# Kernel optimization log

Hardware: AMD Instinct MI355X
Metric: run time of the kernel (lower is better)

## Reference

```python
import jax, jax.numpy as jnp
import numpy as np

B, T, D, E = 8, 512, 128, 256

def setup_inputs() -> dict:
    key = jax.random.key(0)
    ks = jax.random.split(key, 6)
    s_d = 1.0 / np.sqrt(D)
    return {
        "x": jax.random.normal(ks[0], (B, T, D), jnp.float32),
        "Wg": jax.random.normal(ks[1], (D, E), jnp.float32) * s_d,
        "bg": jnp.zeros((E,), jnp.float32),
        "expert_w": jax.random.normal(ks[2], (E, D, D), jnp.float32) * s_d,
        "w1": jax.random.normal(ks[3], (D, D), jnp.float32) * s_d,
        "b1": jnp.zeros((D,), jnp.float32),
        "w2": jax.random.normal(ks[4], (D, D), jnp.float32) * s_d,
        "b2": jnp.zeros((D,), jnp.float32),
    }

def reference(x, Wg, bg, expert_w, w1, b1, w2, b2):
    n_experts = expert_w.shape[0]
    # router (context=None -> route on x itself)
    gate_scores = jax.nn.softmax(x @ Wg + bg, axis=-1)            # [B,T,E]
    top_vals, top_idx = jax.lax.top_k(gate_scores, 2)             # [B,T,2]
    top_w = top_vals / (jnp.sum(top_vals, axis=-1, keepdims=True) + 1e-6)
    # dense per-expert projection (faithful to original einsum over ALL experts)
    expert_outputs = jnp.einsum('btd,edo->bteo', x, expert_w)     # [B,T,E,D]
    # top-2 one-hot mask with normalized weights -> [B,T,E]
    mask = jnp.sum(jax.nn.one_hot(top_idx, n_experts, dtype=x.dtype) * top_w[..., None], axis=2)
    mixed = jnp.einsum('bteo,bte->bto', expert_outputs, mask)     # [B,T,D]
    # SwiGLU
    g = mixed @ w1 + b1
    weighted_avg = g * jax.nn.sigmoid(g) * (mixed @ w2 + b2)      # [B,T,D]
    # variance consensus against swiglu output
    diff_sq = jnp.square(expert_outputs - weighted_avg[:, :, None, :])
    weighted_var = jnp.einsum('bteo,bte->bto', diff_sq, mask)     # [B,T,D]
    consensus = jnp.exp(-jnp.mean(weighted_var, axis=-1))         # [B,T]
    return weighted_avg, consensus
```

## Files before the change

### kernel.cpp

```cpp
#include <hip/hip_runtime.h>
#include <math.h>

#define NT  4096
#define DD  128
#define EE  256
#define CAP 2048

__global__ __launch_bounds__(256) void logits_kernel(
    const float* __restrict__ x, const float* __restrict__ Wg,
    const float* __restrict__ bg, float* __restrict__ logits,
    int* __restrict__ cnt)
{
    const int bid = blockIdx.x;
    const int tid = threadIdx.x;
    if (bid == 0) cnt[tid] = 0;

    __shared__ float xt[DD][8];

    {
        const int q = tid >> 5, part = tid & 31;
        const float4 v = *(reinterpret_cast<const float4*>(
            x + (size_t)(bid * 8 + q) * DD) + part);
        xt[part * 4 + 0][q] = v.x;
        xt[part * 4 + 1][q] = v.y;
        xt[part * 4 + 2][q] = v.z;
        xt[part * 4 + 3][q] = v.w;
    }
    __syncthreads();

    const int e = tid;
    const float be = bg[e];
    float a0 = be, a1 = be, a2 = be, a3 = be;
    float a4 = be, a5 = be, a6 = be, a7 = be;
    #pragma unroll 8
    for (int d = 0; d < DD; ++d) {
        const float w = Wg[(size_t)d * EE + e];
        const float4 xa = *reinterpret_cast<const float4*>(&xt[d][0]);
        const float4 xb = *reinterpret_cast<const float4*>(&xt[d][4]);
        a0 = fmaf(xa.x, w, a0);  a1 = fmaf(xa.y, w, a1);
        a2 = fmaf(xa.z, w, a2);  a3 = fmaf(xa.w, w, a3);
        a4 = fmaf(xb.x, w, a4);  a5 = fmaf(xb.y, w, a5);
        a6 = fmaf(xb.z, w, a6);  a7 = fmaf(xb.w, w, a7);
    }
    float* lr = logits + (size_t)(bid * 8) * EE + e;
    lr[0 * EE] = a0;  lr[1 * EE] = a1;  lr[2 * EE] = a2;  lr[3 * EE] = a3;
    lr[4 * EE] = a4;  lr[5 * EE] = a5;  lr[6 * EE] = a6;  lr[7 * EE] = a7;
}

__global__ __launch_bounds__(256) void top2_kernel(
    const float* __restrict__ logits, float2* __restrict__ w_out,
    int* __restrict__ cnt, int* __restrict__ plist)
{
    const int lane = threadIdx.x & 63;
    const int t    = blockIdx.x * 4 + (threadIdx.x >> 6);
    const float4 lg = *reinterpret_cast<const float4*>(logits + (size_t)t * EE + lane * 4);
    float v[4] = {lg.x, lg.y, lg.z, lg.w};

    float m = v[0]; int mi = lane * 4;
    #pragma unroll
    for (int j = 1; j < 4; ++j)
        if (v[j] > m) { m = v[j]; mi = lane * 4 + j; }
    #pragma unroll
    for (int s = 32; s; s >>= 1) {
        const float om = __shfl_xor(m, s);
        const int   oi = __shfl_xor(mi, s);
        if (om > m || (om == m && oi < mi)) { m = om; mi = oi; }
    }

    float ssum = 0.0f;
    #pragma unroll
    for (int j = 0; j < 4; ++j) ssum += __expf(v[j] - m);
    #pragma unroll
    for (int s = 32; s; s >>= 1) ssum += __shfl_xor(ssum, s);

    float m2 = -INFINITY; int mi2 = 0;
    #pragma unroll
    for (int j = 0; j < 4; ++j) {
        const int ei = lane * 4 + j;
        if (ei != mi && v[j] > m2) { m2 = v[j]; mi2 = ei; }
    }
    #pragma unroll
    for (int s = 32; s; s >>= 1) {
        const float om = __shfl_xor(m2, s);
        const int   oi = __shfl_xor(mi2, s);
        if (om > m2 || (om == m2 && oi < mi2)) { m2 = om; mi2 = oi; }
    }

    if (lane == 0) {
        const float p1 = 1.0f / ssum;
        const float p2 = __expf(m2 - m) / ssum;
        const float den = p1 + p2 + 1e-6f;
        w_out[t] = make_float2(p1 / den, p2 / den);
        const int pos1 = atomicAdd(&cnt[mi], 1);
        if (pos1 < CAP) plist[mi * CAP + pos1] = t * 2;
        const int pos2 = atomicAdd(&cnt[mi2], 1);
        if (pos2 < CAP) plist[mi2 * CAP + pos2] = t * 2 + 1;
    }
}

__global__ __launch_bounds__(128) void expert_kernel(
    const float* __restrict__ x, const float* __restrict__ ew,
    const int* __restrict__ cnt, const int* __restrict__ plist,
    float* __restrict__ ybuf)
{
    const int wg = (blockIdx.x & 7) * 256 + (blockIdx.x >> 3);
    const int e  = wg >> 3;
    const int c  = wg & 7;
    int n = cnt[e];
    if (n > CAP) n = CAP;
    if (n <= c) return;

    const int o   = threadIdx.x;
    const int* pl = plist + e * CAP;
    const float* W = ew + (size_t)e * DD * DD;

    __shared__ float xt[DD][8];
    __shared__ int   fis[8];

    for (int base = c; base < n; base += 64) {
        {
            const int q = o >> 4, part = o & 15;
            if (base + q * 8 < n) {
                const int fi = pl[base + q * 8];
                if (part == 0) fis[q] = fi;
                const float4* xr = reinterpret_cast<const float4*>(
                    x + (size_t)(fi >> 1) * DD) + part * 2;
                const float4 u0 = xr[0], u1 = xr[1];
                xt[part * 8 + 0][q] = u0.x;  xt[part * 8 + 1][q] = u0.y;
                xt[part * 8 + 2][q] = u0.z;  xt[part * 8 + 3][q] = u0.w;
                xt[part * 8 + 4][q] = u1.x;  xt[part * 8 + 5][q] = u1.y;
                xt[part * 8 + 6][q] = u1.z;  xt[part * 8 + 7][q] = u1.w;
            }
        }
        __syncthreads();

        float a0 = 0.f, a1 = 0.f, a2 = 0.f, a3 = 0.f;
        float a4 = 0.f, a5 = 0.f, a6 = 0.f, a7 = 0.f;
        #pragma unroll 8
        for (int d = 0; d < DD; ++d) {
            const float w = W[(size_t)d * DD + o];
            const float4 xa = *reinterpret_cast<const float4*>(&xt[d][0]);
            const float4 xb = *reinterpret_cast<const float4*>(&xt[d][4]);
            a0 = fmaf(xa.x, w, a0);  a1 = fmaf(xa.y, w, a1);
            a2 = fmaf(xa.z, w, a2);  a3 = fmaf(xa.w, w, a3);
            a4 = fmaf(xb.x, w, a4);  a5 = fmaf(xb.y, w, a5);
            a6 = fmaf(xb.z, w, a6);  a7 = fmaf(xb.w, w, a7);
        }

        if (base + 0 * 8 < n) ybuf[(size_t)fis[0] * DD + o] = a0;
        if (base + 1 * 8 < n) ybuf[(size_t)fis[1] * DD + o] = a1;
        if (base + 2 * 8 < n) ybuf[(size_t)fis[2] * DD + o] = a2;
        if (base + 3 * 8 < n) ybuf[(size_t)fis[3] * DD + o] = a3;
        if (base + 4 * 8 < n) ybuf[(size_t)fis[4] * DD + o] = a4;
        if (base + 5 * 8 < n) ybuf[(size_t)fis[5] * DD + o] = a5;
        if (base + 6 * 8 < n) ybuf[(size_t)fis[6] * DD + o] = a6;
        if (base + 7 * 8 < n) ybuf[(size_t)fis[7] * DD + o] = a7;
        __syncthreads();
    }
}

__global__ __launch_bounds__(256) void swiglu_kernel(
    const float* __restrict__ ybuf, const float2* __restrict__ ww,
    const float* __restrict__ w1, const float* __restrict__ b1,
    const float* __restrict__ w2, const float* __restrict__ b2,
    float* __restrict__ out_avg, float* __restrict__ out_cons)
{
    const int o     = threadIdx.x & 127;
    const int which = threadIdx.x >> 7;
    const int t0    = blockIdx.x * 4;
    const float* Wc  = which ? w2 : w1;
    const float bias = which ? b2[o] : b1[o];
    float wreg[DD];
    #pragma unroll
    for (int d = 0; d < DD; ++d) wreg[d] = Wc[d * DD + o];

    __shared__ float ms[DD];
    __shared__ float hs[DD];
    __shared__ float vred[2];

    for (int tk = 0; tk < 4; ++tk) {
        const int t = t0 + tk;
        const float2 w = ww[t];
        const float ya = ybuf[(size_t)(2 * t) * DD + o];
        const float yb = ybuf[(size_t)(2 * t + 1) * DD + o];
        const float mx = w.x * ya + w.y * yb;
        if (!which) ms[o] = mx;
        __syncthreads();

        float acc = bias;
        #pragma unroll
        for (int d0 = 0; d0 < DD; d0 += 4) {
            const float4 mv = *reinterpret_cast<const float4*>(ms + d0);
            acc = fmaf(mv.x, wreg[d0 + 0], acc);
            acc = fmaf(mv.y, wreg[d0 + 1], acc);
            acc = fmaf(mv.z, wreg[d0 + 2], acc);
            acc = fmaf(mv.w, wreg[d0 + 3], acc);
        }
        if (which) hs[o] = acc;
        __syncthreads();

        if (!which) {
            const float g   = acc, hv = hs[o];
            const float sig = 1.0f / (1.0f + __expf(-g));
            const float wavg = g * sig * hv;
            out_avg[(size_t)t * DD + o] = wavg;
            const float da = ya - wavg, db = yb - wavg;
            float v = w.x * da * da + w.y * db * db;
            #pragma unroll
            for (int s = 32; s; s >>= 1) v += __shfl_down(v, s);
            if ((o & 63) == 0) vred[o >> 6] = v;
        }
        __syncthreads();
        if (threadIdx.x == 0)
            out_cons[t] = __expf(-(vred[0] + vred[1]) * (1.0f / DD));
        __syncthreads();
    }
}

extern "C" void kernel_launch(void* const* d_in, const int* in_sizes, int n_in,
                              void* d_out, int out_size, void* d_ws, size_t ws_size,
                              hipStream_t stream) {
    const float* x   = (const float*)d_in[0];
    const float* Wg  = (const float*)d_in[1];
    const float* bg  = (const float*)d_in[2];
    const float* ew  = (const float*)d_in[3];
    const float* w1  = (const float*)d_in[4];
    const float* b1  = (const float*)d_in[5];
    const float* w2  = (const float*)d_in[6];
    const float* b2  = (const float*)d_in[7];

    float* out_avg  = (float*)d_out;
    float* out_cons = out_avg + (size_t)NT * DD;

    char* ws = (char*)d_ws;
    float*  logits = (float*)ws;
    float*  ybuf   = logits;
    float2* wwp    = (float2*)(ws + 4 * 1024 * 1024);
    int*    cnt    = (int*)   (ws + 4 * 1024 * 1024 + 32 * 1024);
    int*    plist  = (int*)   (ws + 4 * 1024 * 1024 + 64 * 1024);

    logits_kernel<<<NT / 8, 256, 0, stream>>>(x, Wg, bg, logits, cnt);
    top2_kernel  <<<NT / 4, 256, 0, stream>>>(logits, wwp, cnt, plist);
    expert_kernel<<<EE * 8, 128, 0, stream>>>(x, ew, cnt, plist, ybuf);
    swiglu_kernel<<<NT / 4, 256, 0, stream>>>(ybuf, wwp, w1, b1, w2, b2,
                                              out_avg, out_cons);
}
```

Before: 60.14 us.

## Restructure SwiGLU kernel to process 8 tokens per block with register blocking

The SwiGLU kernel no longer preloads a full 128-float weight column into registers and walks 4 tokens sequentially with several barriers per token. Each block now stages 8 mixed token vectors transposed in shared memory. Each thread computes 8 token outputs at once, streaming weights from global memory, so every weight load is reused 8 times. The epilogue uses float4 loads and stores with a 32-lane shuffle reduction per token, which cuts register pressure and syncs. The cost is that weights are reread from global or cache per block rather than held in registers, and ybuf is read twice.

```diff
diff --git a/kernel.cpp b/kernel.cpp
--- a/kernel.cpp
+++ b/kernel.cpp
@@ -165,55 +165,89 @@
     const float* __restrict__ w2, const float* __restrict__ b2,
     float* __restrict__ out_avg, float* __restrict__ out_cons)
 {
-    const int o     = threadIdx.x & 127;
-    const int which = threadIdx.x >> 7;
-    const int t0    = blockIdx.x * 4;
-    const float* Wc  = which ? w2 : w1;
-    const float bias = which ? b2[o] : b1[o];
-    float wreg[DD];
-    #pragma unroll
-    for (int d = 0; d < DD; ++d) wreg[d] = Wc[d * DD + o];
-
-    __shared__ float ms[DD];
-    __shared__ float hs[DD];
-    __shared__ float vred[2];
-
-    for (int tk = 0; tk < 4; ++tk) {
-        const int t = t0 + tk;
+    const int tid = threadIdx.x;
+    const int t0  = blockIdx.x * 8;
+
+    __shared__ float mt[DD][8];
+    __shared__ float gh[2][8][DD];
+
+    {
+        const int q = tid >> 5, part = tid & 31;
+        const int t = t0 + q;
         const float2 w = ww[t];
-        const float ya = ybuf[(size_t)(2 * t) * DD + o];
-        const float yb = ybuf[(size_t)(2 * t + 1) * DD + o];
-        const float mx = w.x * ya + w.y * yb;
-        if (!which) ms[o] = mx;
-        __syncthreads();
-
-        float acc = bias;
+        const float4 a = *(reinterpret_cast<const float4*>(
+            ybuf + (size_t)(2 * t) * DD) + part);
+        const float4 b = *(reinterpret_cast<const float4*>(
+            ybuf + (size_t)(2 * t + 1) * DD) + part);
+        mt[part * 4 + 0][q] = w.x * a.x + w.y * b.x;
+        mt[part * 4 + 1][q] = w.x * a.y + w.y * b.y;
+        mt[part * 4 + 2][q] = w.x * a.z + w.y * b.z;
+        mt[part * 4 + 3][q] = w.x * a.w + w.y * b.w;
+    }
+    __syncthreads();
+
+    {
+        const int o = tid & 127, h = tid >> 7;
+        const float* Wc = h ? w2 : w1;
+        const float bias = h ? b2[o] : b1[o];
+        float a0 = bias, a1 = bias, a2 = bias, a3 = bias;
+        float a4 = bias, a5 = bias, a6 = bias, a7 = bias;
+        #pragma unroll 8
+        for (int d = 0; d < DD; ++d) {
+            const float w = Wc[(size_t)d * DD + o];
+            const float4 xa = *reinterpret_cast<const float4*>(&mt[d][0]);
+            const float4 xb = *reinterpret_cast<const float4*>(&mt[d][4]);
+            a0 = fmaf(xa.x, w, a0);  a1 = fmaf(xa.y, w, a1);
+            a2 = fmaf(xa.z, w, a2);  a3 = fmaf(xa.w, w, a3);
+            a4 = fmaf(xb.x, w, a4);  a5 = fmaf(xb.y, w, a5);
+            a6 = fmaf(xb.z, w, a6);  a7 = fmaf(xb.w, w, a7);
+        }
+        gh[h][0][o] = a0;  gh[h][1][o] = a1;  gh[h][2][o] = a2;  gh[h][3][o] = a3;
+        gh[h][4][o] = a4;  gh[h][5][o] = a5;  gh[h][6][o] = a6;  gh[h][7][o] = a7;
+    }
+    __syncthreads();
+
+    {
+        const int q = tid >> 5, part = tid & 31;
+        const int t = t0 + q;
+        const float2 w = ww[t];
+        const float4 a = *(reinterpret_cast<const float4*>(
+            ybuf + (size_t)(2 * t) * DD) + part);
+        const float4 b = *(reinterpret_cast<const float4*>(
+            ybuf + (size_t)(2 * t + 1) * DD) + part);
+        const float4 gv = *reinterpret_cast<const float4*>(&gh[0][q][part * 4]);
+        const float4 hv = *reinterpret_cast<const float4*>(&gh[1][q][part * 4]);
+
+        float4 r; float v = 0.0f;
+        {
+            const float g = gv.x, sig = 1.0f / (1.0f + __expf(-g));
+            r.x = g * sig * hv.x;
+            const float da = a.x - r.x, db = b.x - r.x;
+            v += w.x * da * da + w.y * db * db;
+        }
+        {
+            const float g = gv.y, sig = 1.0f / (1.0f + __expf(-g));
+            r.y = g * sig * hv.y;
+            const float da = a.y - r.y, db = b.y - r.y;
+            v += w.x * da * da + w.y * db * db;
+        }
+        {
+            const float g = gv.z, sig = 1.0f / (1.0f + __expf(-g));
+            r.z = g * sig * hv.z;
+            const float da = a.z - r.z, db = b.z - r.z;
+            v += w.x * da * da + w.y * db * db;
+        }
+        {
+            const float g = gv.w, sig = 1.0f / (1.0f + __expf(-g));
+            r.w = g * sig * hv.w;
+            const float da = a.w - r.w, db = b.w - r.w;
+            v += w.x * da * da + w.y * db * db;
+        }
+        *(reinterpret_cast<float4*>(out_avg + (size_t)t * DD) + part) = r;
+
         #pragma unroll
-        for (int d0 = 0; d0 < DD; d0 += 4) {
-            const float4 mv = *reinterpret_cast<const float4*>(ms + d0);
-            acc = fmaf(mv.x, wreg[d0 + 0], acc);
-            acc = fmaf(mv.y, wreg[d0 + 1], acc);
-            acc = fmaf(mv.z, wreg[d0 + 2], acc);
-            acc = fmaf(mv.w, wreg[d0 + 3], acc);
-        }
-        if (which) hs[o] = acc;
-        __syncthreads();
-
-        if (!which) {
-            const float g   = acc, hv = hs[o];
-            const float sig = 1.0f / (1.0f + __expf(-g));
-            const float wavg = g * sig * hv;
-            out_avg[(size_t)t * DD + o] = wavg;
-            const float da = ya - wavg, db = yb - wavg;
-            float v = w.x * da * da + w.y * db * db;
-            #pragma unroll
-            for (int s = 32; s; s >>= 1) v += __shfl_down(v, s);
-            if ((o & 63) == 0) vred[o >> 6] = v;
-        }
-        __syncthreads();
-        if (threadIdx.x == 0)
-            out_cons[t] = __expf(-(vred[0] + vred[1]) * (1.0f / DD));
-        __syncthreads();
+        for (int s = 16; s; s >>= 1) v += __shfl_down(v, s);
+        if (part == 0) out_cons[t] = __expf(-v * (1.0f / DD));
     }
 }
 
@@ -242,6 +276,6 @@
     logits_kernel<<<NT / 8, 256, 0, stream>>>(x, Wg, bg, logits, cnt);
     top2_kernel  <<<NT / 4, 256, 0, stream>>>(logits, wwp, cnt, plist);
     expert_kernel<<<EE * 8, 128, 0, stream>>>(x, ew, cnt, plist, ybuf);
-    swiglu_kernel<<<NT / 4, 256, 0, stream>>>(ybuf, wwp, w1, b1, w2, b2,
+    swiglu_kernel<<<NT / 8, 256, 0, stream>>>(ybuf, wwp, w1, b1, w2, b2,
                                               out_avg, out_cons);
 }
```

Result: faster. 52.74 us (-12.3%).
